# Kernel tuning notes

Hardware: AMD Instinct MI355X
Metric: run time of the kernel (lower is better)

Reference implementation:

```python
import jax, jax.numpy as jnp
import numpy as np

CHANNELS = 1024
T_LEN = 16384
WINDOW = 16
W_MIN, W_MAX = -1.0, 3.0
BETA = 0.95       # snn.Leaky(beta=0.95)
THRESHOLD = 1.0   # snn.Leaky(threshold=1)


def setup_inputs() -> dict:
    key = jax.random.key(0)
    inp = jax.random.normal(key, (CHANNELS, T_LEN), dtype=jnp.float32)
    return {"inp": inp}


def reference(inp):
    C, T = inp.shape
    pad = WINDOW // 2
    inp_padded = jnp.pad(inp, ((0, 0), (pad, pad)))  # [C, T + WINDOW]
    n_steps = T - WINDOW

    def step(carry, t):
        w, mem = carry
        # B: sliding window [C, WINDOW] starting at column t of padded input
        B = jax.lax.dynamic_slice(inp_padded, (0, t), (C, WINDOW))
        # mean(B @ B.T, axis=1) == B @ mean(B, axis=0)  -- avoids [C, C] intermediate
        B_ram = B @ jnp.mean(B, axis=0)
        w = jnp.clip(0.5 * w + 0.5 * B_ram, W_MIN, W_MAX)
        x = B[:, 0]  # == inp_padded[:, t]
        # snntorch Leaky, reset_mechanism='subtract':
        # reset from incoming mem, then mem = beta*mem + input - reset*thr, spk = mem > thr
        reset = (mem > THRESHOLD).astype(inp.dtype)
        mem = BETA * mem + w * x - reset * THRESHOLD
        spk = (mem > THRESHOLD).astype(inp.dtype)
        return (w, mem), spk

    w0 = jnp.ones((C,), dtype=inp.dtype)
    mem0 = jnp.zeros((C,), dtype=inp.dtype)
    _, spks = jax.lax.scan(step, (w0, mem0), jnp.arange(n_steps))  # spks: [n_steps, C]
    # out = deepcopy(inp); out[:, t] = spk for t < T - WINDOW
    out = inp.at[:, :n_steps].set(spks.T)
    return out
```

## Files before the change

### kernel.cpp

```cpp
#include <hip/hip_runtime.h>

#define C_CH   1024
#define T_DIM  16384
#define NSTEPS (T_DIM - 16)
#define PAD    8
#define TP     (T_DIM + 16)
#define CHUNK  256
#define NCHUNK 64
#define WARM   256

#define WS_CM_OFFSET (8u * T_DIM * sizeof(double))

__global__ void colsum_partial(const float* __restrict__ inp, double* __restrict__ part) {
    int col4 = (blockIdx.x * 256 + threadIdx.x) * 4;
    int rc   = blockIdx.y;
    const float* p = inp + (size_t)rc * 128 * T_DIM + col4;
    double ax = 0.0, ay = 0.0, az = 0.0, aw = 0.0;
    #pragma unroll 4
    for (int r = 0; r < 128; ++r) {
        float4 v = *(const float4*)(p + (size_t)r * T_DIM);
        ax += (double)v.x; ay += (double)v.y; az += (double)v.z; aw += (double)v.w;
    }
    double* q = part + (size_t)rc * T_DIM + col4;
    q[0] = ax; q[1] = ay; q[2] = az; q[3] = aw;
}

__global__ void colmean_tail(const double* __restrict__ part, const float* __restrict__ inp,
                             float* __restrict__ cm, float* __restrict__ out) {
    int i = blockIdx.x * 256 + threadIdx.x;
    if (i < TP) {
        float v = 0.0f;
        if (i >= PAD && i < T_DIM + PAD) {
            int col = i - PAD;
            double t = 0.0;
            #pragma unroll
            for (int r = 0; r < 8; ++r) t += part[(size_t)r * T_DIM + col];
            v = (float)(t * (1.0 / 1024.0));
        }
        cm[i] = v;
    }
    if (i < C_CH * 16) {
        int c = i >> 4, j = i & 15;
        size_t idx = (size_t)c * T_DIM + NSTEPS + j;
        out[idx] = inp[idx];
    }
}

__global__ __launch_bounds__(64) void scan_kernel(const float* __restrict__ inp,
                                                  const float* __restrict__ cm,
                                                  float* __restrict__ out) {
    const int k  = blockIdx.x;
    const int c  = blockIdx.y * 64 + threadIdx.x;
    const int t0 = k * CHUNK;
    const int tend = min(t0 + CHUNK, NSTEPS);
    const int tw = (k == 0) ? 0 : t0 - WARM;

    const float* row  = inp + (size_t)c * T_DIM;
    float*       orow = out + (size_t)c * T_DIM;

    float xs[16], ms[16];
    float win = 0.0f;
    #pragma unroll
    for (int j = 0; j < 16; ++j) {
        int s = tw + j;
        float x = (s >= PAD) ? row[s - PAD] : 0.0f;
        float m = cm[s];
        xs[j] = x; ms[j] = m;
        win = fmaf(x, m, win);
    }

    float w = 1.0f, mem = 0.0f;

    float4 a0 = *(const float4*)(row + tw + 8);
    float4 a1 = *(const float4*)(row + tw + 12);
    float4 a2 = *(const float4*)(row + tw + 16);
    float4 a3 = *(const float4*)(row + tw + 20);
    float4 b0 = *(const float4*)(cm + tw + 16);
    float4 b1 = *(const float4*)(cm + tw + 20);
    float4 b2 = *(const float4*)(cm + tw + 24);
    float4 b3 = *(const float4*)(cm + tw + 28);

    for (int t = tw; t < tend; t += 16) {
        float xn[16] = {a0.x,a0.y,a0.z,a0.w, a1.x,a1.y,a1.z,a1.w,
                        a2.x,a2.y,a2.z,a2.w, a3.x,a3.y,a3.z,a3.w};
        float mn[16] = {b0.x,b0.y,b0.z,b0.w, b1.x,b1.y,b1.z,b1.w,
                        b2.x,b2.y,b2.z,b2.w, b3.x,b3.y,b3.z,b3.w};

        int ts = (t + 16 < tend) ? (t + 16) : t;
        a0 = *(const float4*)(row + ts + 8);
        a1 = *(const float4*)(row + ts + 12);
        a2 = *(const float4*)(row + ts + 16);
        a3 = *(const float4*)(row + ts + 20);
        b0 = *(const float4*)(cm + ts + 16);
        b1 = *(const float4*)(cm + ts + 20);
        b2 = *(const float4*)(cm + ts + 24);
        b3 = *(const float4*)(cm + ts + 28);

        float spk[16];
        #pragma unroll
        for (int j = 0; j < 16; ++j) {
            w = fminf(fmaxf(fmaf(0.5f, w, 0.5f * win), -1.0f), 3.0f);
            float x = xs[j];
            float r = (mem > 1.0f) ? 1.0f : 0.0f;
            mem = fmaf(0.95f, mem, fmaf(w, x, -r));
            spk[j] = (mem > 1.0f) ? 1.0f : 0.0f;
            win = fmaf(xn[j], mn[j], fmaf(-x, ms[j], win));
            xs[j] = xn[j]; ms[j] = mn[j];
        }

        if (t >= t0) {
            *(float4*)(orow + t)      = make_float4(spk[0],  spk[1],  spk[2],  spk[3]);
            *(float4*)(orow + t + 4)  = make_float4(spk[4],  spk[5],  spk[6],  spk[7]);
            *(float4*)(orow + t + 8)  = make_float4(spk[8],  spk[9],  spk[10], spk[11]);
            *(float4*)(orow + t + 12) = make_float4(spk[12], spk[13], spk[14], spk[15]);
        }
    }
}

extern "C" void kernel_launch(void* const* d_in, const int* in_sizes, int n_in,
                              void* d_out, int out_size, void* d_ws, size_t ws_size,
                              hipStream_t stream) {
    const float* inp = (const float*)d_in[0];
    float* out = (float*)d_out;
    double* part = (double*)d_ws;
    float* cm = (float*)((char*)d_ws + WS_CM_OFFSET);

    colsum_partial<<<dim3(T_DIM / 1024, 8), 256, 0, stream>>>(inp, part);
    colmean_tail<<<dim3(65), 256, 0, stream>>>(part, inp, cm, out);
    scan_kernel<<<dim3(NCHUNK, C_CH / 64), 64, 0, stream>>>(inp, cm, out);
}
```

Before: 154.8 us.

## Coalesce scan loads/stores via LDS transpose and halve chunk size

The scan kernel now loads input rows cooperatively, with 4 lanes per row reading float4 segments, and stages the 64x16 tile in padded shared memory so each lane reads its own channel's values. Spikes are written to LDS and stored back with the same coalesced pattern. The column-mean is read directly from global memory each step instead of being kept in a register ring. Chunk size drops to 128 with 128 chunks, which doubles parallelism but keeps a 256-step warmup, so redundant warmup work roughly doubles relative to useful work. Three __syncthreads per 16-step iteration add synchronisation overhead.

After: 172.2 us. 11.2% more time.

```diff
diff --git a/kernel.cpp b/kernel.cpp
--- a/kernel.cpp
+++ b/kernel.cpp
@@ -5,9 +5,11 @@
 #define NSTEPS (T_DIM - 16)
 #define PAD    8
 #define TP     (T_DIM + 16)
-#define CHUNK  256
-#define NCHUNK 64
+#define CHUNK  128
+#define NCHUNK 128
 #define WARM   256
+#define XPADW  21
+#define SPADW  21
 
 #define WS_CM_OFFSET (8u * T_DIM * sizeof(double))
 
@@ -49,71 +51,79 @@
 __global__ __launch_bounds__(64) void scan_kernel(const float* __restrict__ inp,
                                                   const float* __restrict__ cm,
                                                   float* __restrict__ out) {
-    const int k  = blockIdx.x;
-    const int c  = blockIdx.y * 64 + threadIdx.x;
-    const int t0 = k * CHUNK;
+    __shared__ float xt[64][XPADW];
+    __shared__ float st[64][SPADW];
+
+    const int k    = blockIdx.x;
+    const int lane = threadIdx.x;
+    const int c0   = blockIdx.y * 64;
+    const int t0   = k * CHUNK;
     const int tend = min(t0 + CHUNK, NSTEPS);
-    const int tw = (k == 0) ? 0 : t0 - WARM;
+    const int tw   = (t0 - WARM > 0) ? (t0 - WARM) : 0;
 
-    const float* row  = inp + (size_t)c * T_DIM;
-    float*       orow = out + (size_t)c * T_DIM;
+    const float* row = inp + (size_t)(c0 + lane) * T_DIM;
 
-    float xs[16], ms[16];
+    const int sr  = lane >> 2;
+    const int sc4 = (lane & 3) << 2;
+    const float* srow0 = inp + (size_t)(c0 + sr)      * T_DIM + sc4 + 8;
+    const float* srow1 = inp + (size_t)(c0 + sr + 16) * T_DIM + sc4 + 8;
+    const float* srow2 = inp + (size_t)(c0 + sr + 32) * T_DIM + sc4 + 8;
+    const float* srow3 = inp + (size_t)(c0 + sr + 48) * T_DIM + sc4 + 8;
+    float* orow0 = out + (size_t)(c0 + sr)      * T_DIM + sc4;
+    float* orow1 = out + (size_t)(c0 + sr + 16) * T_DIM + sc4;
+    float* orow2 = out + (size_t)(c0 + sr + 32) * T_DIM + sc4;
+    float* orow3 = out + (size_t)(c0 + sr + 48) * T_DIM + sc4;
+
+    float xs[16];
     float win = 0.0f;
     #pragma unroll
     for (int j = 0; j < 16; ++j) {
         int s = tw + j;
         float x = (s >= PAD) ? row[s - PAD] : 0.0f;
-        float m = cm[s];
-        xs[j] = x; ms[j] = m;
-        win = fmaf(x, m, win);
+        xs[j] = x;
+        win = fmaf(x, cm[s], win);
     }
 
     float w = 1.0f, mem = 0.0f;
 
-    float4 a0 = *(const float4*)(row + tw + 8);
-    float4 a1 = *(const float4*)(row + tw + 12);
-    float4 a2 = *(const float4*)(row + tw + 16);
-    float4 a3 = *(const float4*)(row + tw + 20);
-    float4 b0 = *(const float4*)(cm + tw + 16);
-    float4 b1 = *(const float4*)(cm + tw + 20);
-    float4 b2 = *(const float4*)(cm + tw + 24);
-    float4 b3 = *(const float4*)(cm + tw + 28);
+    float4 r0 = *(const float4*)(srow0 + tw);
+    float4 r1 = *(const float4*)(srow1 + tw);
+    float4 r2 = *(const float4*)(srow2 + tw);
+    float4 r3 = *(const float4*)(srow3 + tw);
 
     for (int t = tw; t < tend; t += 16) {
-        float xn[16] = {a0.x,a0.y,a0.z,a0.w, a1.x,a1.y,a1.z,a1.w,
-                        a2.x,a2.y,a2.z,a2.w, a3.x,a3.y,a3.z,a3.w};
-        float mn[16] = {b0.x,b0.y,b0.z,b0.w, b1.x,b1.y,b1.z,b1.w,
-                        b2.x,b2.y,b2.z,b2.w, b3.x,b3.y,b3.z,b3.w};
+        xt[sr][sc4+0]    = r0.x; xt[sr][sc4+1]    = r0.y; xt[sr][sc4+2]    = r0.z; xt[sr][sc4+3]    = r0.w;
+        xt[sr+16][sc4+0] = r1.x; xt[sr+16][sc4+1] = r1.y; xt[sr+16][sc4+2] = r1.z; xt[sr+16][sc4+3] = r1.w;
+        xt[sr+32][sc4+0] = r2.x; xt[sr+32][sc4+1] = r2.y; xt[sr+32][sc4+2] = r2.z; xt[sr+32][sc4+3] = r2.w;
+        xt[sr+48][sc4+0] = r3.x; xt[sr+48][sc4+1] = r3.y; xt[sr+48][sc4+2] = r3.z; xt[sr+48][sc4+3] = r3.w;
+        __syncthreads();
 
         int ts = (t + 16 < tend) ? (t + 16) : t;
-        a0 = *(const float4*)(row + ts + 8);
-        a1 = *(const float4*)(row + ts + 12);
-        a2 = *(const float4*)(row + ts + 16);
-        a3 = *(const float4*)(row + ts + 20);
-        b0 = *(const float4*)(cm + ts + 16);
-        b1 = *(const float4*)(cm + ts + 20);
-        b2 = *(const float4*)(cm + ts + 24);
-        b3 = *(const float4*)(cm + ts + 28);
+        r0 = *(const float4*)(srow0 + ts);
+        r1 = *(const float4*)(srow1 + ts);
+        r2 = *(const float4*)(srow2 + ts);
+        r3 = *(const float4*)(srow3 + ts);
 
-        float spk[16];
         #pragma unroll
         for (int j = 0; j < 16; ++j) {
             w = fminf(fmaxf(fmaf(0.5f, w, 0.5f * win), -1.0f), 3.0f);
-            float x = xs[j];
-            float r = (mem > 1.0f) ? 1.0f : 0.0f;
-            mem = fmaf(0.95f, mem, fmaf(w, x, -r));
-            spk[j] = (mem > 1.0f) ? 1.0f : 0.0f;
-            win = fmaf(xn[j], mn[j], fmaf(-x, ms[j], win));
-            xs[j] = xn[j]; ms[j] = mn[j];
+            float x   = xs[j];
+            float rst = (mem > 1.0f) ? 1.0f : 0.0f;
+            mem = fmaf(0.95f, mem, fmaf(w, x, -rst));
+            st[lane][j] = (mem > 1.0f) ? 1.0f : 0.0f;
+            float xn = xt[lane][j];
+            win = fmaf(xn, cm[t + 16 + j], fmaf(-x, cm[t + j], win));
+            xs[j] = xn;
         }
+        __syncthreads();
 
         if (t >= t0) {
-            *(float4*)(orow + t)      = make_float4(spk[0],  spk[1],  spk[2],  spk[3]);
-            *(float4*)(orow + t + 4)  = make_float4(spk[4],  spk[5],  spk[6],  spk[7]);
-            *(float4*)(orow + t + 8)  = make_float4(spk[8],  spk[9],  spk[10], spk[11]);
-            *(float4*)(orow + t + 12) = make_float4(spk[12], spk[13], spk[14], spk[15]);
+            *(float4*)(orow0 + t) = make_float4(st[sr][sc4],    st[sr][sc4+1],    st[sr][sc4+2],    st[sr][sc4+3]);
+            *(float4*)(orow1 + t) = make_float4(st[sr+16][sc4], st[sr+16][sc4+1], st[sr+16][sc4+2], st[sr+16][sc4+3]);
+            *(float4*)(orow2 + t) = make_float4(st[sr+32][sc4], st[sr+32][sc4+1], st[sr+32][sc4+2], st[sr+32][sc4+3]);
+            *(float4*)(orow3 + t) = make_float4(st[sr+48][sc4], st[sr+48][sc4+1], st[sr+48][sc4+2], st[sr+48][sc4+3]);
         }
+        __syncthreads();
     }
 }
 
```
